# Kernel optimization log

Hardware: AMD Instinct MI355X
Metric: run time of the kernel (lower is better)

The kernel has to match this reference:

```python
import jax, jax.numpy as jnp
import numpy as np

WH, WW = 7, 7
N = WH * WW
DIM = 256
HEADS = 8
HEAD_DIM = DIM // HEADS
SCALE = HEAD_DIM ** -0.5


def _relative_position_index():
    coords = np.stack(np.meshgrid(np.arange(WH), np.arange(WW), indexing='ij'))  # [2,Wh,Ww]
    cf = coords.reshape(2, -1)                      # [2,N]
    rel = cf[:, :, None] - cf[:, None, :]           # [2,N,N]
    rel = rel.transpose(1, 2, 0)                    # [N,N,2]
    rel[..., 0] += WH - 1
    rel[..., 1] += WW - 1
    rel[..., 0] *= 2 * WW - 1
    return rel.sum(-1)                              # [N,N] in [0, (2Wh-1)(2Ww-1))

_REL_IDX = jnp.asarray(_relative_position_index())


def setup_inputs() -> dict:
    key = jax.random.key(0)
    ks = jax.random.split(key, 6)
    B_ = 8192
    return {
        'x': jax.random.normal(ks[0], (B_, N, DIM), dtype=jnp.float32),
        'qkv_w': jax.random.normal(ks[1], (3 * DIM, DIM), dtype=jnp.float32) * 0.02,
        'qkv_b': jax.random.normal(ks[2], (3 * DIM,), dtype=jnp.float32) * 0.02,
        'proj_w': jax.random.normal(ks[3], (DIM, DIM), dtype=jnp.float32) * 0.02,
        'proj_b': jax.random.normal(ks[4], (DIM,), dtype=jnp.float32) * 0.02,
        'bias_table': jax.random.normal(ks[5], ((2 * WH - 1) * (2 * WW - 1), HEADS), dtype=jnp.float32) * 0.02,
    }


def reference(x, qkv_w, qkv_b, proj_w, proj_b, bias_table):
    B_, n, C = x.shape
    # QKV projection -> [3, B_, H, N, hd]
    qkv = (x @ qkv_w.T + qkv_b).reshape(B_, n, 3, HEADS, HEAD_DIM)
    qkv = jnp.transpose(qkv, (2, 0, 3, 1, 4))
    q, k, v = qkv[0], qkv[1], qkv[2]
    # Gathered relative position bias: [H, N, N]
    bias = bias_table[_REL_IDX.reshape(-1)].reshape(n, n, HEADS).transpose(2, 0, 1)
    # Scaled dot-product attention with additive bias
    attn = jnp.einsum('bhnd,bhmd->bhnm', q, k) * SCALE + bias[None]
    attn = jax.nn.softmax(attn, axis=-1)
    out = jnp.einsum('bhnm,bhmd->bhnd', attn, v)
    out = jnp.transpose(out, (0, 2, 1, 3)).reshape(B_, n, C)
    return out @ proj_w.T + proj_b
```

## Files before the change

### kernel.cpp

```cpp
#include <hip/hip_runtime.h>
#include <hip/hip_bf16.h>
#include <stdint.h>

#define NTOK 49
#define SCALE 0.17677669529663687f
#define LOG2E 1.4426950408889634f

typedef __attribute__((ext_vector_type(8))) short bf16x8;
typedef __attribute__((ext_vector_type(4))) float f32x4;

__device__ __forceinline__ unsigned short f2bf(float f) {
    union { float f; unsigned int u; } v; v.f = f;
    unsigned int r = v.u + 0x7FFFu + ((v.u >> 16) & 1u);
    return (unsigned short)(r >> 16);
}

__device__ __forceinline__ uint32_t pkbf(float lo, float hi) {
    __hip_bfloat162 h = __float22bfloat162_rn(float2{lo, hi});
    union { __hip_bfloat162 h; uint32_t u; } c; c.h = h;
    return c.u;
}

__global__ void prep_kernel(const float* __restrict__ qkv_w,
                            const float* __restrict__ proj_w,
                            const float* __restrict__ bias_table,
                            const float* __restrict__ qkv_b,
                            unsigned short* __restrict__ w_qkv,
                            unsigned short* __restrict__ w_proj,
                            float* __restrict__ bias_p,
                            float* __restrict__ sbias) {
    const int total = 196608 + 65536 + 32768 + 768;
    for (int i = blockIdx.x * blockDim.x + threadIdx.x; i < total;
         i += gridDim.x * blockDim.x) {
        if (i < 196608) {
            float s = (i < 65536) ? SCALE * LOG2E : 1.0f;
            w_qkv[i] = f2bf(qkv_w[i] * s);
        } else if (i < 262144) {
            w_proj[i - 196608] = f2bf(proj_w[i - 196608]);
        } else if (i < 294912) {
            int idx = i - 262144;
            int hh = idx >> 12;
            int j  = (idx >> 6) & 63;
            int ii = idx & 63;
            float v;
            if (j >= NTOK)       v = -1e30f;
            else if (ii >= NTOK) v = 0.0f;
            else {
                int rel = (ii / 7 - j / 7 + 6) * 13 + (ii % 7 - j % 7 + 6);
                v = bias_table[rel * 8 + hh];
            }
            bias_p[hh * 4096 + (j >> 2) * 256 + ii * 4 + (j & 3)] = v * LOG2E;
        } else {
            int r = i - 294912;
            sbias[r] = qkv_b[r] * (r < 256 ? SCALE * LOG2E : 1.0f);
        }
    }
}

__global__ __launch_bounds__(512, 4) void wattn_kernel(
    const float* __restrict__ x,
    const unsigned short* __restrict__ w_qkv,
    const unsigned short* __restrict__ w_proj,
    const float* __restrict__ bias_p,
    const float* __restrict__ sbias,
    const float* __restrict__ proj_b,
    float* __restrict__ out)
{
    extern __shared__ char smem[];
    unsigned short* sX = (unsigned short*)smem;
    unsigned short* scrBase = sX + 64 * 264;

    const int tid  = threadIdx.x;
    const int wv   = tid >> 6;
    const int lane = tid & 63;
    const int l16  = lane & 15;
    const int g    = lane >> 4;
    const int lk   = g * 8;

    unsigned short* scr = scrBase + wv * (64 * 36);
    const int b = blockIdx.x;
    const int h = wv;
    const f32x4 fz = {0.f, 0.f, 0.f, 0.f};

    const float* xb = x + (size_t)b * (NTOK * 256);
    #pragma unroll
    for (int it = 0; it < 3; ++it) {
        const int idx = tid * 8 + it * 4096;
        float4 v0 = *(const float4*)(xb + idx);
        float4 v1 = *(const float4*)(xb + idx + 4);
        int r = idx >> 8, c = idx & 255;
        *(uint4*)(sX + r * 264 + c) = make_uint4(pkbf(v0.x, v0.y), pkbf(v0.z, v0.w),
                                                 pkbf(v1.x, v1.y), pkbf(v1.z, v1.w));
    }
    if (tid < 32) {
        const int idx = 12288 + tid * 8;
        float4 v0 = *(const float4*)(xb + idx);
        float4 v1 = *(const float4*)(xb + idx + 4);
        int r = idx >> 8, c = idx & 255;
        *(uint4*)(sX + r * 264 + c) = make_uint4(pkbf(v0.x, v0.y), pkbf(v0.z, v0.w),
                                                 pkbf(v1.x, v1.y), pkbf(v1.z, v1.w));
    }
    if (tid < 480) {
        const int idx = tid * 8;
        *(uint4*)(sX + (49 + (idx >> 8)) * 264 + (idx & 255)) = make_uint4(0, 0, 0, 0);
    }
    __syncthreads();

    bf16x8 qf[4], kf[4], vf[2][2];

    {
        f32x4 acc[4][4];
        #pragma unroll
        for (int mt = 0; mt < 4; ++mt)
            #pragma unroll
            for (int nt = 0; nt < 4; ++nt) acc[mt][nt] = fz;

        const unsigned short* wp[4];
        wp[0] = w_qkv + (h * 32 + l16) * 256 + lk;
        wp[1] = wp[0] + 16 * 256;
        wp[2] = wp[0] + 256 * 256;
        wp[3] = wp[2] + 16 * 256;

        bf16x8 awc[4], awn[4];
        #pragma unroll
        for (int mt = 0; mt < 4; ++mt) awc[mt] = *(const bf16x8*)(wp[mt]);

        #pragma unroll 1
        for (int kb = 0; kb < 8; ++kb) {
            const int kn = ((kb + 1) & 7) * 32;
            #pragma unroll
            for (int mt = 0; mt < 4; ++mt)
                awn[mt] = *(const bf16x8*)(wp[mt] + kn);
            bf16x8 bx[4];
            #pragma unroll
            for (int nt = 0; nt < 4; ++nt)
                bx[nt] = *(const bf16x8*)(sX + (nt * 16 + l16) * 264 + kb * 32 + lk);
            #pragma unroll
            for (int mt = 0; mt < 4; ++mt)
                #pragma unroll
                for (int nt = 0; nt < 4; ++nt)
                    acc[mt][nt] = __builtin_amdgcn_mfma_f32_16x16x32_bf16(
                        awc[mt], bx[nt], acc[mt][nt], 0, 0, 0);
            #pragma unroll
            for (int mt = 0; mt < 4; ++mt) awc[mt] = awn[mt];
        }

        float4 bq0 = *(const float4*)(sbias + h * 32 + 4 * g);
        float4 bq1 = *(const float4*)(sbias + h * 32 + 16 + 4 * g);
        #pragma unroll
        for (int nt = 0; nt < 4; ++nt) {
            acc[0][nt][0] += bq0.x; acc[0][nt][1] += bq0.y;
            acc[0][nt][2] += bq0.z; acc[0][nt][3] += bq0.w;
            acc[1][nt][0] += bq1.x; acc[1][nt][1] += bq1.y;
            acc[1][nt][2] += bq1.z; acc[1][nt][3] += bq1.w;
        }
        #pragma unroll
        for (int nt = 0; nt < 4; ++nt)
            #pragma unroll
            for (int mt = 0; mt < 2; ++mt) {
                uint2 d = make_uint2(pkbf(acc[mt][nt][0], acc[mt][nt][1]),
                                     pkbf(acc[mt][nt][2], acc[mt][nt][3]));
                *(uint2*)(scr + (nt * 16 + l16) * 36 + mt * 16 + 4 * g) = d;
            }
        #pragma unroll
        for (int nt = 0; nt < 4; ++nt)
            qf[nt] = *(const bf16x8*)(scr + (nt * 16 + l16) * 36 + lk);
        #pragma unroll
        for (int nt = 0; nt < 4; ++nt)
            #pragma unroll
            for (int mt = 2; mt < 4; ++mt) {
                uint2 d = make_uint2(pkbf(acc[mt][nt][0], acc[mt][nt][1]),
                                     pkbf(acc[mt][nt][2], acc[mt][nt][3]));
                *(uint2*)(scr + (nt * 16 + l16) * 36 + (mt - 2) * 16 + 4 * g) = d;
            }
        #pragma unroll
        for (int nt = 0; nt < 4; ++nt)
            kf[nt] = *(const bf16x8*)(scr + (nt * 16 + l16) * 36 + lk);
    }

    {
        f32x4 acc[4][2];
        #pragma unroll
        for (int rt = 0; rt < 4; ++rt) { acc[rt][0] = fz; acc[rt][1] = fz; }

        const unsigned short* vp0 = w_qkv + (512 + h * 32 + l16) * 256 + lk;
        const unsigned short* vp1 = vp0 + 16 * 256;

        bf16x8 bwc[2], bwn[2];
        bwc[0] = *(const bf16x8*)(vp0);
        bwc[1] = *(const bf16x8*)(vp1);

        #pragma unroll 1
        for (int kb = 0; kb < 8; ++kb) {
            const int kn = ((kb + 1) & 7) * 32;
            bwn[0] = *(const bf16x8*)(vp0 + kn);
            bwn[1] = *(const bf16x8*)(vp1 + kn);
            bf16x8 ax[4];
            #pragma unroll
            for (int rt = 0; rt < 4; ++rt)
                ax[rt] = *(const bf16x8*)(sX + (rt * 16 + l16) * 264 + kb * 32 + lk);
            #pragma unroll
            for (int ct = 0; ct < 2; ++ct)
                #pragma unroll
                for (int rt = 0; rt < 4; ++rt)
                    acc[rt][ct] = __builtin_amdgcn_mfma_f32_16x16x32_bf16(
                        ax[rt], bwc[ct], acc[rt][ct], 0, 0, 0);
            bwc[0] = bwn[0]; bwc[1] = bwn[1];
        }
        #pragma unroll
        for (int rt = 0; rt < 4; ++rt)
            #pragma unroll
            for (int ct = 0; ct < 2; ++ct) {
                uint2 d = make_uint2(pkbf(acc[rt][ct][0], acc[rt][ct][1]),
                                     pkbf(acc[rt][ct][2], acc[rt][ct][3]));
                *(uint2*)(scr + ((rt >> 1) * 32 + ct * 16 + l16) * 36 + (rt & 1) * 16 + 4 * g) = d;
            }
        #pragma unroll
        for (int dm = 0; dm < 2; ++dm)
            #pragma unroll
            for (int kk = 0; kk < 2; ++kk)
                vf[dm][kk] = *(const bf16x8*)(scr + (kk * 32 + dm * 16 + l16) * 36 + lk);
    }

    const float* bp_h = bias_p + h * 4096;
    float4 bv0 = *(const float4*)(sbias + 512 + h * 32 + 4 * g);
    float4 bv1 = *(const float4*)(sbias + 512 + h * 32 + 16 + 4 * g);

    uint2 o_st[2][2][2];

    #pragma unroll
    for (int hf = 0; hf < 2; ++hf) {
        f32x4 s[4][2];
        #pragma unroll
        for (int tr = 0; tr < 4; ++tr)
            #pragma unroll
            for (int tl = 0; tl < 2; ++tl) {
                const int i = (hf * 2 + tl) * 16 + l16;
                s[tr][tl] = *(const f32x4*)(bp_h + (tr * 4 + g) * 256 + i * 4);
            }
        __builtin_amdgcn_s_setprio(1);
        #pragma unroll
        for (int tr = 0; tr < 4; ++tr)
            #pragma unroll
            for (int tl = 0; tl < 2; ++tl)
                s[tr][tl] = __builtin_amdgcn_mfma_f32_16x16x32_bf16(
                    kf[tr], qf[hf * 2 + tl], s[tr][tl], 0, 0, 0);
        __builtin_amdgcn_s_setprio(0);

        float inv[2];
        #pragma unroll
        for (int tl = 0; tl < 2; ++tl) {
            float s4[4];
            #pragma unroll
            for (int tr = 0; tr < 4; ++tr) {
                float e0 = __builtin_amdgcn_exp2f(s[tr][tl][0]);
                float e1 = __builtin_amdgcn_exp2f(s[tr][tl][1]);
                float e2 = __builtin_amdgcn_exp2f(s[tr][tl][2]);
                float e3 = __builtin_amdgcn_exp2f(s[tr][tl][3]);
                s[tr][tl][0] = e0; s[tr][tl][1] = e1;
                s[tr][tl][2] = e2; s[tr][tl][3] = e3;
                s4[tr] = (e0 + e1) + (e2 + e3);
            }
            float sum = (s4[0] + s4[1]) + (s4[2] + s4[3]);
            sum += __shfl_xor(sum, 16);
            sum += __shfl_xor(sum, 32);
            inv[tl] = 1.0f / sum;
        }

        #pragma unroll
        for (int tr = 0; tr < 4; ++tr)
            #pragma unroll
            for (int tl = 0; tl < 2; ++tl) {
                uint2 d = make_uint2(pkbf(s[tr][tl][0], s[tr][tl][1]),
                                     pkbf(s[tr][tl][2], s[tr][tl][3]));
                *(uint2*)(scr + ((tr >> 1) * 32 + tl * 16 + l16) * 36 + (tr & 1) * 16 + 4 * g) = d;
            }
        bf16x8 pf[2][2];
        #pragma unroll
        for (int tl = 0; tl < 2; ++tl)
            #pragma unroll
            for (int kk = 0; kk < 2; ++kk)
                pf[tl][kk] = *(const bf16x8*)(scr + (kk * 32 + tl * 16 + l16) * 36 + lk);

        f32x4 o[2][2];
        #pragma unroll
        for (int dm = 0; dm < 2; ++dm) { o[dm][0] = fz; o[dm][1] = fz; }
        __builtin_amdgcn_s_setprio(1);
        #pragma unroll
        for (int dm = 0; dm < 2; ++dm)
            #pragma unroll
            for (int tl = 0; tl < 2; ++tl)
                #pragma unroll
                for (int kk = 0; kk < 2; ++kk)
                    o[dm][tl] = __builtin_amdgcn_mfma_f32_16x16x32_bf16(
                        vf[dm][kk], pf[tl][kk], o[dm][tl], 0, 0, 0);
        __builtin_amdgcn_s_setprio(0);

        #pragma unroll
        for (int dm = 0; dm < 2; ++dm) {
            const float4 bv = dm ? bv1 : bv0;
            #pragma unroll
            for (int tl = 0; tl < 2; ++tl) {
                const float iv = inv[tl];
                float r0 = o[dm][tl][0] * iv + bv.x;
                float r1 = o[dm][tl][1] * iv + bv.y;
                float r2 = o[dm][tl][2] * iv + bv.z;
                float r3 = o[dm][tl][3] * iv + bv.w;
                o_st[hf][dm][tl] = make_uint2(pkbf(r0, r1), pkbf(r2, r3));
            }
        }
    }

    __syncthreads();

    #pragma unroll
    for (int hf = 0; hf < 2; ++hf)
        #pragma unroll
        for (int dm = 0; dm < 2; ++dm)
            #pragma unroll
            for (int tl = 0; tl < 2; ++tl)
                *(uint2*)(sX + ((hf * 2 + tl) * 16 + l16) * 264 + h * 32 + dm * 16 + 4 * g)
                    = o_st[hf][dm][tl];
    __syncthreads();

    {
        f32x4 acc[4][2];
        #pragma unroll
        for (int rt = 0; rt < 4; ++rt) { acc[rt][0] = fz; acc[rt][1] = fz; }

        const unsigned short* pp0 = w_proj + (wv * 32 + l16) * 256 + lk;
        const unsigned short* pp1 = pp0 + 16 * 256;

        bf16x8 bwc[2], bwn[2];
        bwc[0] = *(const bf16x8*)(pp0);
        bwc[1] = *(const bf16x8*)(pp1);

        #pragma unroll 1
        for (int kb = 0; kb < 8; ++kb) {
            const int kn = ((kb + 1) & 7) * 32;
            bwn[0] = *(const bf16x8*)(pp0 + kn);
            bwn[1] = *(const bf16x8*)(pp1 + kn);
            bf16x8 a[4];
            #pragma unroll
            for (int rt = 0; rt < 4; ++rt)
                a[rt] = *(const bf16x8*)(sX + (rt * 16 + l16) * 264 + kb * 32 + lk);
            #pragma unroll
            for (int c = 0; c < 2; ++c)
                #pragma unroll
                for (int rt = 0; rt < 4; ++rt)
                    acc[rt][c] = __builtin_amdgcn_mfma_f32_16x16x32_bf16(
                        a[rt], bwc[c], acc[rt][c], 0, 0, 0);
            bwc[0] = bwn[0]; bwc[1] = bwn[1];
        }
        float* ob = out + (size_t)b * (NTOK * 256);
        #pragma unroll
        for (int c = 0; c < 2; ++c) {
            const int col = wv * 32 + c * 16 + l16;
            const float pb = proj_b[col];
            #pragma unroll
            for (int rt = 0; rt < 3; ++rt)
                #pragma unroll
                for (int r = 0; r < 4; ++r)
                    ob[(rt * 16 + 4 * g + r) * 256 + col] = acc[rt][c][r] + pb;
            if (g == 0) ob[48 * 256 + col] = acc[3][c][0] + pb;
        }
    }
}

extern "C" void kernel_launch(void* const* d_in, const int* in_sizes, int n_in,
                              void* d_out, int out_size, void* d_ws, size_t ws_size,
                              hipStream_t stream) {
    const float* x          = (const float*)d_in[0];
    const float* qkv_w      = (const float*)d_in[1];
    const float* qkv_b      = (const float*)d_in[2];
    const float* proj_w     = (const float*)d_in[3];
    const float* proj_b     = (const float*)d_in[4];
    const float* bias_table = (const float*)d_in[5];

    unsigned short* w_qkv  = (unsigned short*)d_ws;
    unsigned short* w_proj = w_qkv + 196608;
    float*          bias_p = (float*)(w_proj + 65536);
    float*          sbias  = bias_p + 32768;

    prep_kernel<<<288, 256, 0, stream>>>(qkv_w, proj_w, bias_table, qkv_b,
                                         w_qkv, w_proj, bias_p, sbias);

    const int SMEM = (64 * 264 + 8 * 64 * 36) * 2;
    hipFuncSetAttribute(reinterpret_cast<const void*>(wattn_kernel),
                        hipFuncAttributeMaxDynamicSharedMemorySize, SMEM);

    wattn_kernel<<<8192, 512, SMEM, stream>>>(x, w_qkv, w_proj, bias_p, sbias,
                                              proj_b, (float*)d_out);
}
```

Before: 588.1 us.

## Prefetch weights early, peel first k-step, stagger waves, and raise MFMA priority

The first QKV, V and proj weight fragments now load before the X staging and the barriers, so their global latency overlaps other work. The first k-iteration of each GEMM is peeled so it accumulates into zero instead of explicitly zeroed registers, and MFMA blocks are wrapped in s_setprio. Each wave sleeps for a small staggered delay after the X barrier to spread out contention for LDS and global memory. The first-half bias tile is also preloaded before the attention loop. This raises register pressure and adds deliberate idle cycles.

Result: slower. 664.1 us (+12.9%).

```diff
diff --git a/kernel.cpp b/kernel.cpp
--- a/kernel.cpp
+++ b/kernel.cpp
@@ -82,6 +82,15 @@
     const int h = wv;
     const f32x4 fz = {0.f, 0.f, 0.f, 0.f};
 
+    const unsigned short* wp[4];
+    wp[0] = w_qkv + (h * 32 + l16) * 256 + lk;
+    wp[1] = wp[0] + 16 * 256;
+    wp[2] = wp[0] + 256 * 256;
+    wp[3] = wp[2] + 16 * 256;
+    bf16x8 awc[4], awn[4];
+    #pragma unroll
+    for (int mt = 0; mt < 4; ++mt) awc[mt] = *(const bf16x8*)(wp[mt]);
+
     const float* xb = x + (size_t)b * (NTOK * 256);
     #pragma unroll
     for (int it = 0; it < 3; ++it) {
@@ -106,27 +115,36 @@
     }
     __syncthreads();
 
+    {
+        const int st = (blockIdx.x * 5 + wv) & 7;
+        for (int i = 0; i < st; ++i) __builtin_amdgcn_s_sleep(2);
+    }
+
     bf16x8 qf[4], kf[4], vf[2][2];
 
     {
         f32x4 acc[4][4];
-        #pragma unroll
-        for (int mt = 0; mt < 4; ++mt)
-            #pragma unroll
-            for (int nt = 0; nt < 4; ++nt) acc[mt][nt] = fz;
-
-        const unsigned short* wp[4];
-        wp[0] = w_qkv + (h * 32 + l16) * 256 + lk;
-        wp[1] = wp[0] + 16 * 256;
-        wp[2] = wp[0] + 256 * 256;
-        wp[3] = wp[2] + 16 * 256;
-
-        bf16x8 awc[4], awn[4];
-        #pragma unroll
-        for (int mt = 0; mt < 4; ++mt) awc[mt] = *(const bf16x8*)(wp[mt]);
-
+        {
+            #pragma unroll
+            for (int mt = 0; mt < 4; ++mt)
+                awn[mt] = *(const bf16x8*)(wp[mt] + 32);
+            bf16x8 bx[4];
+            #pragma unroll
+            for (int nt = 0; nt < 4; ++nt)
+                bx[nt] = *(const bf16x8*)(sX + (nt * 16 + l16) * 264 + lk);
+            __builtin_amdgcn_s_setprio(1);
+            #pragma unroll
+            for (int mt = 0; mt < 4; ++mt)
+                #pragma unroll
+                for (int nt = 0; nt < 4; ++nt)
+                    acc[mt][nt] = __builtin_amdgcn_mfma_f32_16x16x32_bf16(
+                        awc[mt], bx[nt], fz, 0, 0, 0);
+            __builtin_amdgcn_s_setprio(0);
+            #pragma unroll
+            for (int mt = 0; mt < 4; ++mt) awc[mt] = awn[mt];
+        }
         #pragma unroll 1
-        for (int kb = 0; kb < 8; ++kb) {
+        for (int kb = 1; kb < 8; ++kb) {
             const int kn = ((kb + 1) & 7) * 32;
             #pragma unroll
             for (int mt = 0; mt < 4; ++mt)
@@ -135,15 +153,22 @@
             #pragma unroll
             for (int nt = 0; nt < 4; ++nt)
                 bx[nt] = *(const bf16x8*)(sX + (nt * 16 + l16) * 264 + kb * 32 + lk);
+            __builtin_amdgcn_s_setprio(1);
             #pragma unroll
             for (int mt = 0; mt < 4; ++mt)
                 #pragma unroll
                 for (int nt = 0; nt < 4; ++nt)
                     acc[mt][nt] = __builtin_amdgcn_mfma_f32_16x16x32_bf16(
                         awc[mt], bx[nt], acc[mt][nt], 0, 0, 0);
+            __builtin_amdgcn_s_setprio(0);
             #pragma unroll
             for (int mt = 0; mt < 4; ++mt) awc[mt] = awn[mt];
         }
+
+        const unsigned short* vp0 = w_qkv + (512 + h * 32 + l16) * 256 + lk;
+        const unsigned short* vp1 = vp0 + 16 * 256;
+        bf16x8 bwc0 = *(const bf16x8*)(vp0);
+        bf16x8 bwc1 = *(const bf16x8*)(vp1);
 
         float4 bq0 = *(const float4*)(sbias + h * 32 + 4 * g);
         float4 bq1 = *(const float4*)(sbias + h * 32 + 16 + 4 * g);
@@ -176,53 +201,72 @@
         #pragma unroll
         for (int nt = 0; nt < 4; ++nt)
             kf[nt] = *(const bf16x8*)(scr + (nt * 16 + l16) * 36 + lk);
-    }
-
-    {
-        f32x4 acc[4][2];
-        #pragma unroll
-        for (int rt = 0; rt < 4; ++rt) { acc[rt][0] = fz; acc[rt][1] = fz; }
-
-        const unsigned short* vp0 = w_qkv + (512 + h * 32 + l16) * 256 + lk;
-        const unsigned short* vp1 = vp0 + 16 * 256;
-
-        bf16x8 bwc[2], bwn[2];
-        bwc[0] = *(const bf16x8*)(vp0);
-        bwc[1] = *(const bf16x8*)(vp1);
-
-        #pragma unroll 1
-        for (int kb = 0; kb < 8; ++kb) {
-            const int kn = ((kb + 1) & 7) * 32;
-            bwn[0] = *(const bf16x8*)(vp0 + kn);
-            bwn[1] = *(const bf16x8*)(vp1 + kn);
-            bf16x8 ax[4];
+
+        {
+            f32x4 vacc[4][2];
+            {
+                bf16x8 bwn0 = *(const bf16x8*)(vp0 + 32);
+                bf16x8 bwn1 = *(const bf16x8*)(vp1 + 32);
+                bf16x8 ax[4];
+                #pragma unroll
+                for (int rt = 0; rt < 4; ++rt)
+                    ax[rt] = *(const bf16x8*)(sX + (rt * 16 + l16) * 264 + lk);
+                __builtin_amdgcn_s_setprio(1);
+                #pragma unroll
+                for (int rt = 0; rt < 4; ++rt) {
+                    vacc[rt][0] = __builtin_amdgcn_mfma_f32_16x16x32_bf16(
+                        ax[rt], bwc0, fz, 0, 0, 0);
+                    vacc[rt][1] = __builtin_amdgcn_mfma_f32_16x16x32_bf16(
+                        ax[rt], bwc1, fz, 0, 0, 0);
+                }
+                __builtin_amdgcn_s_setprio(0);
+                bwc0 = bwn0; bwc1 = bwn1;
+            }
+            #pragma unroll 1
+            for (int kb = 1; kb < 8; ++kb) {
+                const int kn = ((kb + 1) & 7) * 32;
+                bf16x8 bwn0 = *(const bf16x8*)(vp0 + kn);
+                bf16x8 bwn1 = *(const bf16x8*)(vp1 + kn);
+                bf16x8 ax[4];
+                #pragma unroll
+                for (int rt = 0; rt < 4; ++rt)
+                    ax[rt] = *(const bf16x8*)(sX + (rt * 16 + l16) * 264 + kb * 32 + lk);
+                __builtin_amdgcn_s_setprio(1);
+                #pragma unroll
+                for (int rt = 0; rt < 4; ++rt) {
+                    vacc[rt][0] = __builtin_amdgcn_mfma_f32_16x16x32_bf16(
+                        ax[rt], bwc0, vacc[rt][0], 0, 0, 0);
+                    vacc[rt][1] = __builtin_amdgcn_mfma_f32_16x16x32_bf16(
+                        ax[rt], bwc1, vacc[rt][1], 0, 0, 0);
+                }
+                __builtin_amdgcn_s_setprio(0);
+                bwc0 = bwn0; bwc1 = bwn1;
+            }
             #pragma unroll
             for (int rt = 0; rt < 4; ++rt)
-                ax[rt] = *(const bf16x8*)(sX + (rt * 16 + l16) * 264 + kb * 32 + lk);
-            #pragma unroll
-            for (int ct = 0; ct < 2; ++ct)
-                #pragma unroll
-                for (int rt = 0; rt < 4; ++rt)
-                    acc[rt][ct] = __builtin_amdgcn_mfma_f32_16x16x32_bf16(
-                        ax[rt], bwc[ct], acc[rt][ct], 0, 0, 0);
-            bwc[0] = bwn[0]; bwc[1] = bwn[1];
-        }
-        #pragma unroll
-        for (int rt = 0; rt < 4; ++rt)
-            #pragma unroll
-            for (int ct = 0; ct < 2; ++ct) {
-                uint2 d = make_uint2(pkbf(acc[rt][ct][0], acc[rt][ct][1]),
-                                     pkbf(acc[rt][ct][2], acc[rt][ct][3]));
-                *(uint2*)(scr + ((rt >> 1) * 32 + ct * 16 + l16) * 36 + (rt & 1) * 16 + 4 * g) = d;
-            }
-        #pragma unroll
-        for (int dm = 0; dm < 2; ++dm)
-            #pragma unroll
-            for (int kk = 0; kk < 2; ++kk)
-                vf[dm][kk] = *(const bf16x8*)(scr + (kk * 32 + dm * 16 + l16) * 36 + lk);
+                #pragma unroll
+                for (int ct = 0; ct < 2; ++ct) {
+                    uint2 d = make_uint2(pkbf(vacc[rt][ct][0], vacc[rt][ct][1]),
+                                         pkbf(vacc[rt][ct][2], vacc[rt][ct][3]));
+                    *(uint2*)(scr + ((rt >> 1) * 32 + ct * 16 + l16) * 36 + (rt & 1) * 16 + 4 * g) = d;
+                }
+            #pragma unroll
+            for (int dm = 0; dm < 2; ++dm)
+                #pragma unroll
+                for (int kk = 0; kk < 2; ++kk)
+                    vf[dm][kk] = *(const bf16x8*)(scr + (kk * 32 + dm * 16 + l16) * 36 + lk);
+        }
     }
 
     const float* bp_h = bias_p + h * 4096;
+
+    f32x4 s0pre[4][2];
+    #pragma unroll
+    for (int tr = 0; tr < 4; ++tr)
+        #pragma unroll
+        for (int tl = 0; tl < 2; ++tl)
+            s0pre[tr][tl] = *(const f32x4*)(bp_h + (tr * 4 + g) * 256 + (tl * 16 + l16) * 4);
+
     float4 bv0 = *(const float4*)(sbias + 512 + h * 32 + 4 * g);
     float4 bv1 = *(const float4*)(sbias + 512 + h * 32 + 16 + 4 * g);
 
@@ -234,10 +278,9 @@
         #pragma unroll
         for (int tr = 0; tr < 4; ++tr)
             #pragma unroll
-            for (int tl = 0; tl < 2; ++tl) {
-                const int i = (hf * 2 + tl) * 16 + l16;
-                s[tr][tl] = *(const f32x4*)(bp_h + (tr * 4 + g) * 256 + i * 4);
-            }
+            for (int tl = 0; tl < 2; ++tl)
+                s[tr][tl] = hf ? *(const f32x4*)(bp_h + (tr * 4 + g) * 256 + ((2 + tl) * 16 + l16) * 4)
+                               : s0pre[tr][tl];
         __builtin_amdgcn_s_setprio(1);
         #pragma unroll
         for (int tr = 0; tr < 4; ++tr)
@@ -283,17 +326,16 @@
                 pf[tl][kk] = *(const bf16x8*)(scr + (kk * 32 + tl * 16 + l16) * 36 + lk);
 
         f32x4 o[2][2];
-        #pragma unroll
-        for (int dm = 0; dm < 2; ++dm) { o[dm][0] = fz; o[dm][1] = fz; }
         __builtin_amdgcn_s_setprio(1);
         #pragma unroll
         for (int dm = 0; dm < 2; ++dm)
             #pragma unroll
-            for (int tl = 0; tl < 2; ++tl)
-                #pragma unroll
-                for (int kk = 0; kk < 2; ++kk)
-                    o[dm][tl] = __builtin_amdgcn_mfma_f32_16x16x32_bf16(
-                        vf[dm][kk], pf[tl][kk], o[dm][tl], 0, 0, 0);
+            for (int tl = 0; tl < 2; ++tl) {
+                o[dm][tl] = __builtin_amdgcn_mfma_f32_16x16x32_bf16(
+                    vf[dm][0], pf[tl][0], fz, 0, 0, 0);
+                o[dm][tl] = __builtin_amdgcn_mfma_f32_16x16x32_bf16(
+                    vf[dm][1], pf[tl][1], o[dm][tl], 0, 0, 0);
+            }
         __builtin_amdgcn_s_setprio(0);
 
         #pragma unroll
@@ -311,6 +353,11 @@
         }
     }
 
+    const unsigned short* pp0 = w_proj + (wv * 32 + l16) * 256 + lk;
+    const unsigned short* pp1 = pp0 + 16 * 256;
+    bf16x8 pwc0 = *(const bf16x8*)(pp0);
+    bf16x8 pwc1 = *(const bf16x8*)(pp1);
+
     __syncthreads();
 
     #pragma unroll
@@ -325,32 +372,43 @@
 
     {
         f32x4 acc[4][2];
-        #pragma unroll
-        for (int rt = 0; rt < 4; ++rt) { acc[rt][0] = fz; acc[rt][1] = fz; }
-
-        const unsigned short* pp0 = w_proj + (wv * 32 + l16) * 256 + lk;
-        const unsigned short* pp1 = pp0 + 16 * 256;
-
-        bf16x8 bwc[2], bwn[2];
-        bwc[0] = *(const bf16x8*)(pp0);
-        bwc[1] = *(const bf16x8*)(pp1);
-
+        {
+            bf16x8 pwn0 = *(const bf16x8*)(pp0 + 32);
+            bf16x8 pwn1 = *(const bf16x8*)(pp1 + 32);
+            bf16x8 a[4];
+            #pragma unroll
+            for (int rt = 0; rt < 4; ++rt)
+                a[rt] = *(const bf16x8*)(sX + (rt * 16 + l16) * 264 + lk);
+            __builtin_amdgcn_s_setprio(1);
+            #pragma unroll
+            for (int rt = 0; rt < 4; ++rt) {
+                acc[rt][0] = __builtin_amdgcn_mfma_f32_16x16x32_bf16(
+                    a[rt], pwc0, fz, 0, 0, 0);
+                acc[rt][1] = __builtin_amdgcn_mfma_f32_16x16x32_bf16(
+                    a[rt], pwc1, fz, 0, 0, 0);
+            }
+            __builtin_amdgcn_s_setprio(0);
+            pwc0 = pwn0; pwc1 = pwn1;
+        }
         #pragma unroll 1
-        for (int kb = 0; kb < 8; ++kb) {
+        for (int kb = 1; kb < 8; ++kb) {
             const int kn = ((kb + 1) & 7) * 32;
-            bwn[0] = *(const bf16x8*)(pp0 + kn);
-            bwn[1] = *(const bf16x8*)(pp1 + kn);
+            bf16x8 pwn0 = *(const bf16x8*)(pp0 + kn);
+            bf16x8 pwn1 = *(const bf16x8*)(pp1 + kn);
             bf16x8 a[4];
             #pragma unroll
             for (int rt = 0; rt < 4; ++rt)
                 a[rt] = *(const bf16x8*)(sX + (rt * 16 + l16) * 264 + kb * 32 + lk);
-            #pragma unroll
-            for (int c = 0; c < 2; ++c)
-                #pragma unroll
-                for (int rt = 0; rt < 4; ++rt)
-                    acc[rt][c] = __builtin_amdgcn_mfma_f32_16x16x32_bf16(
-                        a[rt], bwc[c], acc[rt][c], 0, 0, 0);
-            bwc[0] = bwn[0]; bwc[1] = bwn[1];
+            __builtin_amdgcn_s_setprio(1);
+            #pragma unroll
+            for (int rt = 0; rt < 4; ++rt) {
+                acc[rt][0] = __builtin_amdgcn_mfma_f32_16x16x32_bf16(
+                    a[rt], pwc0, acc[rt][0], 0, 0, 0);
+                acc[rt][1] = __builtin_amdgcn_mfma_f32_16x16x32_bf16(
+                    a[rt], pwc1, acc[rt][1], 0, 0, 0);
+            }
+            __builtin_amdgcn_s_setprio(0);
+            pwc0 = pwn0; pwc1 = pwn1;
         }
         float* ob = out + (size_t)b * (NTOK * 256);
         #pragma unroll
```
